# Kernel optimization log

Measured on AMD Instinct MI355X. Metric: run time of the kernel, lower is better.

## Reference

```python
import jax, jax.numpy as jnp
import numpy as np

D_MODEL = 1024
NUM_BLOCKS = 4

def setup_inputs() -> dict:
    key = jax.random.key(0)
    k1, k2 = jax.random.split(key)
    x = jax.random.normal(k1, (8, 4096, D_MODEL), dtype=jnp.float32)
    # Linear(d_model, d_model) params, torch-style fan_in init scale
    W = jax.random.normal(k2, (D_MODEL, D_MODEL), dtype=jnp.float32) * (1.0 / np.sqrt(D_MODEL))
    b = jnp.zeros((D_MODEL,), dtype=jnp.float32)
    return {"x": x, "W": W, "b": b, "num_blocks": NUM_BLOCKS}

def reference(x, W, b, num_blocks):
    # x: [B, L, D]; split L into num_blocks blocks; SE-style gating per block.
    B, L, D = x.shape
    bs = L // num_blocks
    xb = x.reshape(B, num_blocks, bs, D)          # [B, nb, bs, D]
    pooled = jnp.mean(xb, axis=2)                 # avg-pool over block length -> [B, nb, D]
    gate = jax.nn.sigmoid(jnp.einsum('bnd,ed->bne', pooled, W) + b)  # Linear + sigmoid
    out = xb * gate[:, :, None, :]                # broadcast over block length
    return out.reshape(B, L, D)
```

## Files before the change

### kernel.cpp

```cpp
#include <hip/hip_runtime.h>

#define B    8
#define L    4096
#define D    1024
#define NB   4
#define BS   (L / NB)
#define BN   (B * NB)
#define RS   16
#define ROWS_PER (BS / RS)

__global__ void pool_partial(const float* __restrict__ x, float* __restrict__ partial) {
    int gid = blockIdx.x;
    int s   = gid & (RS - 1);
    int bn  = gid / RS;
    int t   = threadIdx.x;

    const float4* xb = (const float4*)(x + (size_t)bn * BS * D + (size_t)s * ROWS_PER * D);
    float4 acc = make_float4(0.f, 0.f, 0.f, 0.f);
    #pragma unroll 4
    for (int r = 0; r < ROWS_PER; ++r) {
        float4 v = xb[(size_t)r * (D / 4) + t];
        acc.x += v.x; acc.y += v.y; acc.z += v.z; acc.w += v.w;
    }
    float4* p = (float4*)(partial + ((size_t)bn * RS + s) * D);
    p[t] = acc;
}

__global__ void pool_reduce(const float* __restrict__ partial, float* __restrict__ pooled) {
    int bn = blockIdx.x;
    int t  = threadIdx.x;
    const float4* p = (const float4*)(partial + (size_t)bn * RS * D);
    float4 acc = make_float4(0.f, 0.f, 0.f, 0.f);
    #pragma unroll
    for (int s = 0; s < RS; ++s) {
        float4 v = p[(size_t)s * (D / 4) + t];
        acc.x += v.x; acc.y += v.y; acc.z += v.z; acc.w += v.w;
    }
    const float inv = 1.0f / (float)BS;
    float4* o = (float4*)(pooled + (size_t)bn * D);
    o[t] = make_float4(acc.x * inv, acc.y * inv, acc.z * inv, acc.w * inv);
}

__global__ void gate_kernel(const float* __restrict__ pooled, const float* __restrict__ W,
                            const float* __restrict__ bias, float* __restrict__ gate) {
    int blk   = blockIdx.x;
    int bn    = blk >> 4;
    int etile = blk & 15;
    int t     = threadIdx.x;
    int wv    = t >> 6;
    int lane  = t & 63;

    const float4* p4 = (const float4*)(pooled + (size_t)bn * D);

    for (int i = 0; i < 16; ++i) {
        int e = etile * 64 + wv * 16 + i;
        const float4* wr = (const float4*)(W + (size_t)e * D);
        float sum = 0.f;
        #pragma unroll
        for (int c = 0; c < 4; ++c) {
            float4 w = wr[c * 64 + lane];
            float4 p = p4[c * 64 + lane];
            sum += w.x * p.x + w.y * p.y + w.z * p.z + w.w * p.w;
        }
        #pragma unroll
        for (int off = 32; off; off >>= 1) sum += __shfl_down(sum, off);
        if (lane == 0) {
            sum += bias[e];
            gate[(size_t)bn * D + e] = 1.0f / (1.0f + __expf(-sum));
        }
    }
}

__global__ void apply_gate(const float* __restrict__ x, const float* __restrict__ gate,
                           float* __restrict__ out) {
    const size_t total4 = (size_t)B * L * D / 4;
    const float4* x4 = (const float4*)x;
    const float4* g4 = (const float4*)gate;
    float4* o4 = (float4*)out;

    for (size_t f = (size_t)blockIdx.x * blockDim.x + threadIdx.x; f < total4;
         f += (size_t)gridDim.x * blockDim.x) {
        size_t row = f >> 8;
        int bn = (int)((row >> 12) * NB + ((row >> 10) & (NB - 1)));
        float4 g = g4[(size_t)bn * (D / 4) + (f & 255)];
        float4 v = x4[f];
        o4[f] = make_float4(v.x * g.x, v.y * g.y, v.z * g.z, v.w * g.w);
    }
}

extern "C" void kernel_launch(void* const* d_in, const int* in_sizes, int n_in,
                              void* d_out, int out_size, void* d_ws, size_t ws_size,
                              hipStream_t stream) {
    const float* x    = (const float*)d_in[0];
    const float* W    = (const float*)d_in[1];
    const float* bias = (const float*)d_in[2];
    float* out        = (float*)d_out;

    float* partial = (float*)d_ws;
    float* pooled  = partial + (size_t)BN * RS * D;
    float* gate    = pooled + (size_t)BN * D;

    hipLaunchKernelGGL(pool_partial, dim3(BN * RS), dim3(256), 0, stream, x, partial);
    hipLaunchKernelGGL(pool_reduce,  dim3(BN),      dim3(256), 0, stream, partial, pooled);
    hipLaunchKernelGGL(gate_kernel,  dim3(BN * 16), dim3(256), 0, stream, pooled, W, bias, gate);
    hipLaunchKernelGGL(apply_gate,   dim3(4096),    dim3(256), 0, stream, x, gate, out);
}
```

Measured before the change: 274.5 us.

## Fuse pool reduction into gate kernel and widen pooling split

Removes the separate pool_reduce launch by having each gate block reduce the partial sums into shared memory itself, then compute four output rows per iteration with pooled values held in registers. The pooling split count is raised from 16 to 64 to launch more blocks over x. The cost is redundant reduction of partials (8 blocks per bn each read 64×1024 floats) and a larger partial buffer, in exchange for one fewer launch and more memory-level parallelism in the pooling pass.

```diff
diff --git a/kernel.cpp b/kernel.cpp
--- a/kernel.cpp
+++ b/kernel.cpp
@@ -1,72 +1,86 @@
 #include <hip/hip_runtime.h>
 
-#define B    8
-#define L    4096
-#define D    1024
-#define NB   4
-#define BS   (L / NB)
-#define BN   (B * NB)
-#define RS   16
-#define ROWS_PER (BS / RS)
+#define B      8
+#define L      4096
+#define D      1024
+#define NB     4
+#define BS     (L / NB)
+#define BN     (B * NB)
+#define SPLITS 64
+#define ROWS_PER (BS / SPLITS)
 
 __global__ void pool_partial(const float* __restrict__ x, float* __restrict__ partial) {
     int gid = blockIdx.x;
-    int s   = gid & (RS - 1);
-    int bn  = gid / RS;
+    int s   = gid & (SPLITS - 1);
+    int bn  = gid >> 6;
     int t   = threadIdx.x;
 
     const float4* xb = (const float4*)(x + (size_t)bn * BS * D + (size_t)s * ROWS_PER * D);
     float4 acc = make_float4(0.f, 0.f, 0.f, 0.f);
-    #pragma unroll 4
+    #pragma unroll
     for (int r = 0; r < ROWS_PER; ++r) {
         float4 v = xb[(size_t)r * (D / 4) + t];
         acc.x += v.x; acc.y += v.y; acc.z += v.z; acc.w += v.w;
     }
-    float4* p = (float4*)(partial + ((size_t)bn * RS + s) * D);
+    float4* p = (float4*)(partial + ((size_t)bn * SPLITS + s) * D);
     p[t] = acc;
 }
 
-__global__ void pool_reduce(const float* __restrict__ partial, float* __restrict__ pooled) {
-    int bn = blockIdx.x;
-    int t  = threadIdx.x;
-    const float4* p = (const float4*)(partial + (size_t)bn * RS * D);
+__global__ void gate_kernel(const float* __restrict__ partial, const float* __restrict__ W,
+                            const float* __restrict__ bias, float* __restrict__ gate) {
+    __shared__ float4 pool_s[D / 4];
+
+    int blk = blockIdx.x;
+    int bn  = blk >> 3;
+    int et  = blk & 7;
+    int t   = threadIdx.x;
+
+    const float4* p = (const float4*)(partial + (size_t)bn * SPLITS * D);
     float4 acc = make_float4(0.f, 0.f, 0.f, 0.f);
     #pragma unroll
-    for (int s = 0; s < RS; ++s) {
+    for (int s = 0; s < SPLITS; ++s) {
         float4 v = p[(size_t)s * (D / 4) + t];
         acc.x += v.x; acc.y += v.y; acc.z += v.z; acc.w += v.w;
     }
     const float inv = 1.0f / (float)BS;
-    float4* o = (float4*)(pooled + (size_t)bn * D);
-    o[t] = make_float4(acc.x * inv, acc.y * inv, acc.z * inv, acc.w * inv);
-}
+    pool_s[t] = make_float4(acc.x * inv, acc.y * inv, acc.z * inv, acc.w * inv);
+    __syncthreads();
 
-__global__ void gate_kernel(const float* __restrict__ pooled, const float* __restrict__ W,
-                            const float* __restrict__ bias, float* __restrict__ gate) {
-    int blk   = blockIdx.x;
-    int bn    = blk >> 4;
-    int etile = blk & 15;
-    int t     = threadIdx.x;
-    int wv    = t >> 6;
-    int lane  = t & 63;
+    int wv   = t >> 6;
+    int lane = t & 63;
 
-    const float4* p4 = (const float4*)(pooled + (size_t)bn * D);
+    float4 pf[4];
+    #pragma unroll
+    for (int c = 0; c < 4; ++c) pf[c] = pool_s[c * 64 + lane];
 
-    for (int i = 0; i < 16; ++i) {
-        int e = etile * 64 + wv * 16 + i;
-        const float4* wr = (const float4*)(W + (size_t)e * D);
-        float sum = 0.f;
+    int ebase = et * 128 + wv * 32;
+    for (int i = 0; i < 32; i += 4) {
+        float s0 = 0.f, s1 = 0.f, s2 = 0.f, s3 = 0.f;
         #pragma unroll
         for (int c = 0; c < 4; ++c) {
-            float4 w = wr[c * 64 + lane];
-            float4 p = p4[c * 64 + lane];
-            sum += w.x * p.x + w.y * p.y + w.z * p.z + w.w * p.w;
+            float4 w0 = ((const float4*)(W + (size_t)(ebase + i + 0) * D))[c * 64 + lane];
+            float4 w1 = ((const float4*)(W + (size_t)(ebase + i + 1) * D))[c * 64 + lane];
+            float4 w2 = ((const float4*)(W + (size_t)(ebase + i + 2) * D))[c * 64 + lane];
+            float4 w3 = ((const float4*)(W + (size_t)(ebase + i + 3) * D))[c * 64 + lane];
+            float4 pp = pf[c];
+            s0 += w0.x * pp.x + w0.y * pp.y + w0.z * pp.z + w0.w * pp.w;
+            s1 += w1.x * pp.x + w1.y * pp.y + w1.z * pp.z + w1.w * pp.w;
+            s2 += w2.x * pp.x + w2.y * pp.y + w2.z * pp.z + w2.w * pp.w;
+            s3 += w3.x * pp.x + w3.y * pp.y + w3.z * pp.z + w3.w * pp.w;
         }
         #pragma unroll
-        for (int off = 32; off; off >>= 1) sum += __shfl_down(sum, off);
+        for (int off = 32; off; off >>= 1) {
+            s0 += __shfl_down(s0, off);
+            s1 += __shfl_down(s1, off);
+            s2 += __shfl_down(s2, off);
+            s3 += __shfl_down(s3, off);
+        }
         if (lane == 0) {
-            sum += bias[e];
-            gate[(size_t)bn * D + e] = 1.0f / (1.0f + __expf(-sum));
+            int e = ebase + i;
+            gate[(size_t)bn * D + e + 0] = 1.0f / (1.0f + __expf(-(s0 + bias[e + 0])));
+            gate[(size_t)bn * D + e + 1] = 1.0f / (1.0f + __expf(-(s1 + bias[e + 1])));
+            gate[(size_t)bn * D + e + 2] = 1.0f / (1.0f + __expf(-(s2 + bias[e + 2])));
+            gate[(size_t)bn * D + e + 3] = 1.0f / (1.0f + __expf(-(s3 + bias[e + 3])));
         }
     }
 }
@@ -97,11 +111,9 @@
     float* out        = (float*)d_out;
 
     float* partial = (float*)d_ws;
-    float* pooled  = partial + (size_t)BN * RS * D;
-    float* gate    = pooled + (size_t)BN * D;
+    float* gate    = partial + (size_t)BN * SPLITS * D;
 
-    hipLaunchKernelGGL(pool_partial, dim3(BN * RS), dim3(256), 0, stream, x, partial);
-    hipLaunchKernelGGL(pool_reduce,  dim3(BN),      dim3(256), 0, stream, partial, pooled);
-    hipLaunchKernelGGL(gate_kernel,  dim3(BN * 16), dim3(256), 0, stream, pooled, W, bias, gate);
-    hipLaunchKernelGGL(apply_gate,   dim3(4096),    dim3(256), 0, stream, x, gate, out);
+    hipLaunchKernelGGL(pool_partial, dim3(BN * SPLITS), dim3(256), 0, stream, x, partial);
+    hipLaunchKernelGGL(gate_kernel,  dim3(BN * 8),      dim3(256), 0, stream, partial, W, bias, gate);
+    hipLaunchKernelGGL(apply_gate,   dim3(4096),        dim3(256), 0, stream, x, gate, out);
 }
```

Result: slower. 288.8 us (+5.2%).
